# Kernel optimization log

Measured on AMD Instinct MI355X. Metric: run time of the kernel, lower is better.

Reference implementation:

```python
import jax, jax.numpy as jnp
import numpy as np

B, T, C = 8, 1024, 192


def _cluster_one(D, num_clusters):
    """Average-linkage agglomerative clustering on a precomputed [T,T] distance
    matrix (same algorithm as sklearn AgglomerativeClustering(metric='precomputed',
    linkage='average')). Returns int labels in [0, num_clusters)."""
    Tn = D.shape[0]
    INF = jnp.float32(1e9)
    eye = jnp.eye(Tn, dtype=bool)

    def body(_, state):
        D, labels, sizes, active = state
        mask = active[:, None] & active[None, :] & (~eye)
        Dm = jnp.where(mask, D, INF)
        flat = jnp.argmin(Dm)            # closest active pair
        i, j = flat // Tn, flat % Tn     # merge cluster j into cluster i
        ni, nj = sizes[i], sizes[j]
        # average linkage: d(i∪j, k) = (ni*d(i,k) + nj*d(j,k)) / (ni+nj)
        new_row = (ni * D[i] + nj * D[j]) / (ni + nj)
        D = D.at[i, :].set(new_row).at[:, i].set(new_row)
        sizes = sizes.at[i].set(ni + nj)
        active = active.at[j].set(False)
        labels = jnp.where(labels == j, i, labels)
        return (D, labels, sizes, active)

    state0 = (D,
              jnp.arange(Tn),
              jnp.ones((Tn,), jnp.float32),
              jnp.ones((Tn,), bool))
    n_merges = Tn - num_clusters  # static Python int -> static trip count
    D, labels, sizes, active = jax.lax.fori_loop(0, n_merges, body, state0)
    # compact representative indices to labels 0..num_clusters-1 (ordered by rep index)
    reps_sorted = jnp.sort(jnp.where(active, jnp.arange(Tn), Tn))
    return jnp.searchsorted(reps_sorted, labels)


def setup_inputs() -> dict:
    key = jax.random.key(0)
    x = jax.random.normal(key, (B, T, C), dtype=jnp.float32)
    return {"x": x, "num_clusters": 196}


def reference(x, num_clusters):
    num_clusters = min(int(num_clusters), x.shape[1])  # protected = 0
    xn = x / jnp.linalg.norm(x, axis=-1, keepdims=True)
    dist = 1.0 - jnp.einsum('btc,bsc->bts', xn, xn)    # [B,T,T] cosine distance
    labels = jax.vmap(lambda d: _cluster_one(d, num_clusters))(dist)
    return dist, labels
```

## Files before the change

### kernel.cpp

```cpp
#include <hip/hip_runtime.h>
#include <stdint.h>

#define TN 1024
#define CD 192
#define NB 8
#define WPB 16
#define NWG (NB * WPB)
#define NCLUST 196
#define NMERGE (TN - NCLUST)
#define TAILN 168
#define PCAP 64
#define NROUNDS 16
#define HIMASK 0xFFFFFFFF00000000ull

typedef unsigned long long ull;

__device__ __forceinline__ uint32_t f2sort(float f) {
    uint32_t u = __float_as_uint(f);
    return u ^ ((u >> 31) ? 0xFFFFFFFFu : 0x80000000u);
}

template<int CTRL>
__device__ __forceinline__ ull dpp_min64(ull x) {
    int lo = (int)(uint32_t)x, hi = (int)(uint32_t)(x >> 32);
    int tlo = __builtin_amdgcn_update_dpp(lo, lo, CTRL, 0xF, 0xF, false);
    int thi = __builtin_amdgcn_update_dpp(hi, hi, CTRL, 0xF, 0xF, false);
    ull t = ((ull)(uint32_t)thi << 32) | (uint32_t)tlo;
    return (t < x) ? t : x;
}
__device__ __forceinline__ ull wmin64_all(ull x) {
    x = dpp_min64<0x111>(x); x = dpp_min64<0x112>(x);
    x = dpp_min64<0x114>(x); x = dpp_min64<0x118>(x);
    x = dpp_min64<0x142>(x); x = dpp_min64<0x143>(x);
    int lo = __builtin_amdgcn_readlane((int)(uint32_t)x, 63);
    int hi = __builtin_amdgcn_readlane((int)(uint32_t)(x >> 32), 63);
    return ((ull)(uint32_t)hi << 32) | (uint32_t)lo;
}

__global__ void norm_kernel(const float* __restrict__ x, float* __restrict__ xn) {
    int row = blockIdx.x;
    int t = threadIdx.x;
    __shared__ float ssum[4];
    float v = 0.f;
    if (t < CD) v = x[(size_t)row * CD + t];
    float s = v * v;
    #pragma unroll
    for (int off = 32; off > 0; off >>= 1) s += __shfl_xor(s, off, 64);
    if ((t & 63) == 0) ssum[t >> 6] = s;
    __syncthreads();
    float tot = ssum[0] + ssum[1] + ssum[2] + ssum[3];
    float nrm = __fsqrt_rn(tot);
    if (t < CD) xn[(size_t)row * CD + t] = __fdiv_rn(v, nrm);
}

#define KC 32
__global__ __launch_bounds__(256) void dist_kernel(const float* __restrict__ xn,
                                                   float* __restrict__ dout) {
    int b = blockIdx.z;
    int bm = blockIdx.y, bn = blockIdx.x;
    const float* X = xn + (size_t)b * TN * CD;
    __shared__ float As[KC][68];
    __shared__ float Bs[KC][68];
    int tid = threadIdx.x;
    int tx = tid & 15, ty = tid >> 4;
    int lr = tid >> 2;
    int lq = tid & 3;
    float acc[4][4];
    #pragma unroll
    for (int r = 0; r < 4; ++r)
        #pragma unroll
        for (int c = 0; c < 4; ++c) acc[r][c] = 0.f;

    for (int kc = 0; kc < CD; kc += KC) {
        float4 a0 = *(const float4*)&X[(size_t)(bm * 64 + lr) * CD + kc + lq * 4];
        float4 a1 = *(const float4*)&X[(size_t)(bm * 64 + lr) * CD + kc + (lq + 4) * 4];
        float4 b0 = *(const float4*)&X[(size_t)(bn * 64 + lr) * CD + kc + lq * 4];
        float4 b1 = *(const float4*)&X[(size_t)(bn * 64 + lr) * CD + kc + (lq + 4) * 4];
        __syncthreads();
        As[lq * 4 + 0][lr] = a0.x; As[lq * 4 + 1][lr] = a0.y;
        As[lq * 4 + 2][lr] = a0.z; As[lq * 4 + 3][lr] = a0.w;
        As[lq * 4 + 16][lr] = a1.x; As[lq * 4 + 17][lr] = a1.y;
        As[lq * 4 + 18][lr] = a1.z; As[lq * 4 + 19][lr] = a1.w;
        Bs[lq * 4 + 0][lr] = b0.x; Bs[lq * 4 + 1][lr] = b0.y;
        Bs[lq * 4 + 2][lr] = b0.z; Bs[lq * 4 + 3][lr] = b0.w;
        Bs[lq * 4 + 16][lr] = b1.x; Bs[lq * 4 + 17][lr] = b1.y;
        Bs[lq * 4 + 18][lr] = b1.z; Bs[lq * 4 + 19][lr] = b1.w;
        __syncthreads();
        #pragma unroll
        for (int kk = 0; kk < KC; ++kk) {
            float4 av = *(const float4*)&As[kk][ty * 4];
            float4 bv = *(const float4*)&Bs[kk][tx * 4];
            acc[0][0] += av.x * bv.x; acc[0][1] += av.x * bv.y;
            acc[0][2] += av.x * bv.z; acc[0][3] += av.x * bv.w;
            acc[1][0] += av.y * bv.x; acc[1][1] += av.y * bv.y;
            acc[1][2] += av.y * bv.z; acc[1][3] += av.y * bv.w;
            acc[2][0] += av.z * bv.x; acc[2][1] += av.z * bv.y;
            acc[2][2] += av.z * bv.z; acc[2][3] += av.z * bv.w;
            acc[3][0] += av.w * bv.x; acc[3][1] += av.w * bv.y;
            acc[3][2] += av.w * bv.z; acc[3][3] += av.w * bv.w;
        }
    }
    size_t obase = (size_t)b * TN * TN;
    #pragma unroll
    for (int r = 0; r < 4; ++r) {
        int mrow = bm * 64 + ty * 4 + r;
        float4 o;
        o.x = 1.0f - acc[r][0]; o.y = 1.0f - acc[r][1];
        o.z = 1.0f - acc[r][2]; o.w = 1.0f - acc[r][3];
        size_t idx = obase + (size_t)mrow * TN + bn * 64 + tx * 4;
        *(float4*)&dout[idx] = o;
    }
}

__global__ __launch_bounds__(1024)
void init_kernel(const float* __restrict__ Dist, ull* __restrict__ rkg2,
                 float* __restrict__ szg2, int* __restrict__ gidg2,
                 ull* __restrict__ mkg, int* __restrict__ metag2) {
    int b = blockIdx.x >> 4;
    int w = blockIdx.x & 15;
    int k = threadIdx.x;
    int lane = k & 63, wv = k >> 6;
    int gw = w * 16 + wv;
    const float* D0 = Dist + (size_t)b * TN * TN;
    for (int r = gw; r < TN; r += 256) {
        const float* Rr = D0 + (size_t)r * TN;
        ull best = ~0ull;
        for (int s = lane; s < TN; s += 64)
            if (s != r) {
                ull key = ((ull)f2sort(Rr[s]) << 32) | (uint32_t)s;
                if (key < best) best = key;
            }
        best = wmin64_all(best);
        if (lane == 0) rkg2[(size_t)b * TN + r] = best;
    }
    if (w == 0) {
        szg2[b * TN + k] = 1.0f;
        gidg2[b * TN + k] = k;
        mkg[(size_t)b * TN + k] = ~0ull;
        if (k == 0) {
            metag2[b * 4 + 0] = TN;
            metag2[b * 4 + 1] = 0;
            metag2[b * 4 + 2] = 0;
        }
    }
}

__global__ __launch_bounds__(1024)
void round_kernel(int round, const float* __restrict__ Dinit,
                  float* __restrict__ DA, float* __restrict__ DB,
                  ull* __restrict__ rkg2, float* __restrict__ szg2,
                  int* __restrict__ gidg2, ull* __restrict__ mkg,
                  int* __restrict__ metag2) {
    int wg = blockIdx.x;
    int b = wg % NB;
    int w = wg / NB;
    int k = threadIdx.x;
    int lane = k & 63, wv = k >> 6;
    int gw = w * 16 + wv;
    int par = round & 1;

    const int* meta = metag2 + par * NB * 4 + b * 4;
    int N = meta[0], nm = meta[1], which = meta[2];

    if (N <= TAILN) {
        if (w == 0) {
            if (k < N) {
                szg2[(par ^ 1) * NB * TN + b * TN + k] = szg2[par * NB * TN + b * TN + k];
                gidg2[(par ^ 1) * NB * TN + b * TN + k] = gidg2[par * NB * TN + b * TN + k];
            }
            if (k == 0) {
                int* m2 = metag2 + (par ^ 1) * NB * 4 + b * 4;
                m2[0] = N; m2[1] = nm; m2[2] = which;
            }
        }
        return;
    }

    __shared__ ull rk_s[TN];
    __shared__ float sz_s[TN];
    __shared__ int gid_s[TN];
    __shared__ int ts_s[TN];
    __shared__ int n2o_s[TN];
    __shared__ unsigned char dead_s[TN];
    __shared__ int pi_t[512], pj_t[512];
    __shared__ ull pk_t[512];
    __shared__ int spi_s[512], spj_s[512];
    __shared__ int wcnt[16], woffp[16];
    __shared__ int npair_s;

    if (k < N) {
        rk_s[k] = rkg2[(size_t)par * NB * TN + (size_t)b * TN + k];
        sz_s[k] = szg2[par * NB * TN + b * TN + k];
        gid_s[k] = gidg2[par * NB * TN + b * TN + k];
    }
    ts_s[k] = -1;
    dead_s[k] = 0;
    __syncthreads();

    bool mut = false; int cpart = 0;
    if (k < N) {
        ull K = rk_s[k];
        int c = (int)(uint32_t)K;
        if ((int)(uint32_t)rk_s[c] == k && k < c) { mut = true; cpart = c; }
    }
    ull bm = __ballot(mut);
    int lanepre = __popcll(bm & (((ull)1 << lane) - 1ull));
    if (lane == 0) wcnt[wv] = __popcll(bm);
    __syncthreads();
    if (k == 0) {
        int run = 0;
        #pragma unroll
        for (int u = 0; u < 16; ++u) { woffp[u] = run; run += wcnt[u]; }
        npair_s = run;
    }
    __syncthreads();
    if (mut) { int idx = woffp[wv] + lanepre; pi_t[idx] = k; pj_t[idx] = cpart; }
    __syncthreads();
    int np = npair_s;
    if (np == 0) {
        ull cand = ~0ull;
        if (k < N) cand = (rk_s[k] & HIMASK) | (uint32_t)k;
        cand = wmin64_all(cand);
        if (lane == 0) pk_t[wv] = cand;
        __syncthreads();
        if (k == 0) {
            ull g = pk_t[0];
            for (int u = 1; u < 16; ++u) if (pk_t[u] < g) g = pk_t[u];
            int r = (int)(uint32_t)g;
            int c = (int)(uint32_t)rk_s[r];
            pi_t[0] = r < c ? r : c;
            pj_t[0] = r < c ? c : r;
            npair_s = 1;
        }
        __syncthreads();
        np = 1;
    }
    if (k < np) {
        int i = pi_t[k], j = pj_t[k];
        uint32_t vb = (uint32_t)(rk_s[i] >> 32);
        pk_t[k] = ((ull)vb << 20) | ((ull)(uint32_t)gid_s[i] << 10) | (ull)(uint32_t)gid_s[j];
    }
    __syncthreads();
    if (k < np) {
        ull mk = pk_t[k];
        int rank = 0;
        for (int u = 0; u < np; ++u) if (pk_t[u] < mk) ++rank;
        spi_s[rank] = pi_t[k]; spj_s[rank] = pj_t[k];
        if (w == 0) mkg[(size_t)b * TN + nm + rank] = mk;
    }
    __syncthreads();
    if (k < np) { ts_s[spi_s[k]] = k; dead_s[spj_s[k]] = 1; }
    __syncthreads();
    bool alive_ = (k < N) && !dead_s[k];
    ull am = __ballot(alive_);
    int apre = __popcll(am & (((ull)1 << lane) - 1ull));
    if (lane == 0) wcnt[wv] = __popcll(am);
    __syncthreads();
    if (k == 0) {
        int run = 0;
        #pragma unroll
        for (int u = 0; u < 16; ++u) { woffp[u] = run; run += wcnt[u]; }
    }
    __syncthreads();
    if (alive_) n2o_s[woffp[wv] + apre] = k;
    int Nn = N - np;
    __syncthreads();

    const float* cur = (which == 0) ? (Dinit + (size_t)b * TN * TN)
                      : ((which == 1) ? DA : DB) + (size_t)b * TN * TN;
    float* nxt = ((which == 1) ? DB : DA) + (size_t)b * TN * TN;
    int newwhich = (which == 1) ? 2 : 1;

    for (int ap = gw; ap < Nn; ap += 256) {
        int a = n2o_s[ap];
        int qa = ts_s[a];
        float* drow = nxt + (size_t)ap * Nn;
        ull best = ~0ull;
        if (qa < 0) {
            const float* Ra = cur + (size_t)a * N;
            for (int bp = lane; bp < Nn; bp += 64) {
                int bo = n2o_s[bp];
                int qb = ts_s[bo];
                float val;
                if (qb < 0) val = Ra[bo];
                else {
                    int iq = spi_s[qb], jq = spj_s[qb];
                    float niq = sz_s[iq], njq = sz_s[jq];
                    float sq = __fadd_rn(niq, njq);
                    val = __fdiv_rn(__fadd_rn(__fmul_rn(niq, Ra[iq]),
                                              __fmul_rn(njq, Ra[jq])), sq);
                }
                drow[bp] = val;
                if (bp != ap) {
                    ull key = ((ull)f2sort(val) << 32) | (uint32_t)bp;
                    if (key < best) best = key;
                }
            }
        } else {
            int ii = spi_s[qa], jj = spj_s[qa];
            float ni = sz_s[ii], nj = sz_s[jj], ss = __fadd_rn(ni, nj);
            const float* Ri = cur + (size_t)ii * N;
            const float* Rj = cur + (size_t)jj * N;
            for (int bp = lane; bp < Nn; bp += 64) {
                int bo = n2o_s[bp];
                int qb = ts_s[bo];
                float val;
                if (qb < 0) {
                    val = __fdiv_rn(__fadd_rn(__fmul_rn(ni, Ri[bo]),
                                              __fmul_rn(nj, Rj[bo])), ss);
                } else if (qb == qa) {
                    val = 0.0f;
                } else {
                    int p = qa < qb ? qa : qb, q2 = qa < qb ? qb : qa;
                    int ip = spi_s[p], jp = spj_s[p], iq = spi_s[q2], jq = spj_s[q2];
                    float nip = sz_s[ip], njp = sz_s[jp], sp = __fadd_rn(nip, njp);
                    float niq = sz_s[iq], njq = sz_s[jq], sq = __fadd_rn(niq, njq);
                    float t1 = __fdiv_rn(__fadd_rn(__fmul_rn(nip, cur[(size_t)ip * N + iq]),
                                                   __fmul_rn(njp, cur[(size_t)jp * N + iq])), sp);
                    float t2 = __fdiv_rn(__fadd_rn(__fmul_rn(nip, cur[(size_t)ip * N + jq]),
                                                   __fmul_rn(njp, cur[(size_t)jp * N + jq])), sp);
                    val = __fdiv_rn(__fadd_rn(__fmul_rn(niq, t1), __fmul_rn(njq, t2)), sq);
                }
                drow[bp] = val;
                if (bp != ap) {
                    ull key = ((ull)f2sort(val) << 32) | (uint32_t)bp;
                    if (key < best) best = key;
                }
            }
        }
        best = wmin64_all(best);
        if (lane == 0) rkg2[(size_t)(par ^ 1) * NB * TN + (size_t)b * TN + ap] = best;
    }

    if (w == 0) {
        if (k < Nn) {
            int a = n2o_s[k]; int q = ts_s[a];
            float ns = (q >= 0) ? __fadd_rn(sz_s[spi_s[q]], sz_s[spj_s[q]]) : sz_s[a];
            szg2[(par ^ 1) * NB * TN + b * TN + k] = ns;
            gidg2[(par ^ 1) * NB * TN + b * TN + k] = gid_s[a];
        }
        if (k == 0) {
            int* m2 = metag2 + (par ^ 1) * NB * 4 + b * 4;
            m2[0] = Nn; m2[1] = nm + np; m2[2] = newwhich;
        }
    }
}

__global__ __launch_bounds__(1024)
void tail_kernel(int fpar, const float* __restrict__ DA, const float* __restrict__ DB,
                 const float* __restrict__ szg2, const int* __restrict__ gidg2,
                 const ull* __restrict__ mkg, const int* __restrict__ metag2,
                 float* __restrict__ out_labels) {
    int b = blockIdx.x;
    int k = threadIdx.x;
    int lane = k & 63, wv = k >> 6;

    __shared__ float Dl[TAILN * TAILN];
    __shared__ ull rk_s[TAILN];
    __shared__ float sz_s[TAILN];
    __shared__ int gid_s[TAILN];
    __shared__ unsigned char alive[TAILN];
    __shared__ int tsl[TAILN];
    __shared__ float F[PCAP * PCAP];
    __shared__ int pi_t[96], pj_t[96];
    __shared__ ull pk_t[96];
    __shared__ int spi_s[PCAP], spj_s[PCAP];
    __shared__ ull mk_s[TN];
    __shared__ int par_s[TN];
    __shared__ uint32_t rw[32];
    __shared__ int woff2[32];
    __shared__ ull wpA[16];
    __shared__ int npair_s;

    int N = metag2[fpar * NB * 4 + b * 4 + 0];
    int nm = metag2[fpar * NB * 4 + b * 4 + 1];
    int which = metag2[fpar * NB * 4 + b * 4 + 2];
    const float* src = ((which == 1) ? DA : DB) + (size_t)b * TN * TN;

    for (int idx = k; idx < N * N; idx += 1024) Dl[idx] = src[idx];
    mk_s[k] = mkg[(size_t)b * TN + k];
    if (k < N) {
        sz_s[k] = szg2[fpar * NB * TN + b * TN + k];
        gid_s[k] = gidg2[fpar * NB * TN + b * TN + k];
        alive[k] = 1;
        tsl[k] = -1;
    }
    __syncthreads();

    int na = N;
    for (int round = 0; round < 600 && na > 1; ++round) {
        for (int r = wv; r < N; r += 16) {
            ull best = ~0ull;
            if (alive[r]) {
                for (int s = lane; s < N; s += 64)
                    if (alive[s] && s != r) {
                        ull key = ((ull)f2sort(Dl[r * N + s]) << 32) | (uint32_t)s;
                        if (key < best) best = key;
                    }
                best = wmin64_all(best);
            }
            if (lane == 0) rk_s[r] = best;
        }
        if (k == 0) npair_s = 0;
        __syncthreads();
        if (k < N && alive[k]) {
            ull K = rk_s[k];
            int c = (int)(uint32_t)K;
            if ((int)(uint32_t)rk_s[c] == k && k < c) {
                int idx = atomicAdd(&npair_s, 1);
                pi_t[idx] = k; pj_t[idx] = c;
            }
        }
        __syncthreads();
        int np = npair_s;
        if (np == 0) {
            ull cand = ~0ull;
            if (k < N && alive[k]) cand = (rk_s[k] & HIMASK) | (uint32_t)k;
            cand = wmin64_all(cand);
            if (lane == 0) wpA[wv] = cand;
            __syncthreads();
            if (k == 0) {
                ull g = wpA[0];
                for (int u = 1; u < 16; ++u) if (wpA[u] < g) g = wpA[u];
                int r = (int)(uint32_t)g;
                int c = (int)(uint32_t)rk_s[r];
                pi_t[0] = r < c ? r : c;
                pj_t[0] = r < c ? c : r;
                npair_s = 1;
            }
            __syncthreads();
            np = 1;
        }
        int P = np < PCAP ? np : PCAP;
        if (k < np) {
            int i = pi_t[k], j = pj_t[k];
            uint32_t vb = (uint32_t)(rk_s[i] >> 32);
            pk_t[k] = ((ull)vb << 20) | ((ull)(uint32_t)gid_s[i] << 10) | (ull)(uint32_t)gid_s[j];
        }
        __syncthreads();
        if (k < np) {
            ull mk = pk_t[k];
            int rank = 0;
            for (int u = 0; u < np; ++u) if (pk_t[u] < mk) ++rank;
            if (rank < P) { spi_s[rank] = pi_t[k]; spj_s[rank] = pj_t[k]; mk_s[nm + rank] = mk; }
        }
        __syncthreads();
        for (int t = k; t < P * P; t += 1024) {
            int p = t / P, q = t - p * P;
            if (p < q) {
                int ip = spi_s[p], jp = spj_s[p], iq = spi_s[q], jq = spj_s[q];
                float nip = sz_s[ip], njp = sz_s[jp], sp = __fadd_rn(nip, njp);
                float niq = sz_s[iq], njq = sz_s[jq], sq = __fadd_rn(niq, njq);
                float t1 = __fdiv_rn(__fadd_rn(__fmul_rn(nip, Dl[ip * N + iq]),
                                               __fmul_rn(njp, Dl[jp * N + iq])), sp);
                float t2 = __fdiv_rn(__fadd_rn(__fmul_rn(nip, Dl[ip * N + jq]),
                                               __fmul_rn(njp, Dl[jp * N + jq])), sp);
                F[p * PCAP + q] = __fdiv_rn(__fadd_rn(__fmul_rn(niq, t1), __fmul_rn(njq, t2)), sq);
            }
        }
        if (k < P) { tsl[spi_s[k]] = k; alive[spj_s[k]] = 0; }
        __syncthreads();
        for (int q = wv; q < P; q += 16) {
            int ii = spi_s[q], jj = spj_s[q];
            float ni = sz_s[ii], nj = sz_s[jj], ss = __fadd_rn(ni, nj);
            for (int s = lane; s < N; s += 64) {
                if (!alive[s] || s == ii) continue;
                int tp = tsl[s];
                float val;
                if (tp >= 0) {
                    int p2 = tp < q ? tp : q, q2 = tp < q ? q : tp;
                    val = F[p2 * PCAP + q2];
                } else {
                    val = __fdiv_rn(__fadd_rn(__fmul_rn(ni, Dl[ii * N + s]),
                                              __fmul_rn(nj, Dl[jj * N + s])), ss);
                }
                Dl[ii * N + s] = val;
                Dl[s * N + ii] = val;
            }
        }
        __syncthreads();
        if (k < P) {
            int ii = spi_s[k];
            sz_s[ii] = __fadd_rn(sz_s[ii], sz_s[spj_s[k]]);
            tsl[ii] = -1;
        }
        nm += P;
        na -= P;
        __syncthreads();
    }

    __syncthreads();
    par_s[k] = k;
    if (k < 32) rw[k] = 0;
    __syncthreads();
    if (k < TN - 1) {
        ull mk = mk_s[k];
        if (mk != ~0ull) {
            int rank = 0;
            for (int u = 0; u < TN - 1; ++u) if (mk_s[u] < mk) ++rank;
            if (rank < NMERGE) {
                int jj = (int)(mk & 1023ull);
                int ii = (int)((mk >> 10) & 1023ull);
                par_s[jj] = ii;
            }
        }
    }
    __syncthreads();
    #pragma unroll
    for (int it = 0; it < 11; ++it) {
        int p1 = par_s[k];
        int g = par_s[p1];
        __syncthreads();
        par_s[k] = g;
        __syncthreads();
    }
    if (par_s[k] == k) atomicOr(&rw[k >> 5], 1u << (k & 31));
    __syncthreads();
    if (k == 0) {
        int run = 0;
        for (int u = 0; u < 32; ++u) { woff2[u] = run; run += __popc(rw[u]); }
    }
    __syncthreads();
    int p = par_s[k];
    int rank = woff2[p >> 5] + __popc(rw[p >> 5] & ((1u << (p & 31)) - 1u));
    out_labels[(size_t)b * TN + k] = (float)rank;
}

extern "C" void kernel_launch(void* const* d_in, const int* in_sizes, int n_in,
                              void* d_out, int out_size, void* d_ws, size_t ws_size,
                              hipStream_t stream) {
    const float* x = (const float*)d_in[0];
    float* out = (float*)d_out;

    float* xn    = (float*)d_ws;
    float* DAp   = xn + (size_t)NB * TN * CD;
    float* DBp   = DAp + (size_t)NB * TN * TN;
    ull*   rkg2  = (ull*)(DBp + (size_t)NB * TN * TN);
    float* szg2  = (float*)(rkg2 + 2 * (size_t)NB * TN);
    int*   gidg2 = (int*)(szg2 + 2 * (size_t)NB * TN);
    ull*   mkg   = (ull*)(gidg2 + 2 * (size_t)NB * TN);
    int*   metag2 = (int*)(mkg + (size_t)NB * TN);

    float* dist_out   = out;
    float* labels_out = out + (size_t)NB * TN * TN;

    norm_kernel<<<NB * TN, 256, 0, stream>>>(x, xn);
    dim3 g2(16, 16, NB);
    dist_kernel<<<g2, 256, 0, stream>>>(xn, dist_out);
    init_kernel<<<NWG, 1024, 0, stream>>>(dist_out, rkg2, szg2, gidg2, mkg, metag2);
    for (int r = 0; r < NROUNDS; ++r)
        round_kernel<<<NWG, 1024, 0, stream>>>(r, dist_out, DAp, DBp,
                                               rkg2, szg2, gidg2, mkg, metag2);
    tail_kernel<<<NB, 1024, 0, stream>>>(NROUNDS & 1, DAp, DBp, szg2, gidg2,
                                         mkg, metag2, labels_out);
}
```

Measured before the change: 453.7 us.

## Shrink tail threshold and use radix select for merge-key ranking

```diff
diff --git a/kernel.cpp b/kernel.cpp
--- a/kernel.cpp
+++ b/kernel.cpp
@@ -9,8 +9,9 @@
 #define NCLUST 196
 #define NMERGE (TN - NCLUST)
 #define TAILN 168
+#define HSTOP 64
 #define PCAP 64
-#define NROUNDS 16
+#define NROUNDS 14
 #define HIMASK 0xFFFFFFFF00000000ull
 
 typedef unsigned long long ull;
@@ -162,7 +163,7 @@
     const int* meta = metag2 + par * NB * 4 + b * 4;
     int N = meta[0], nm = meta[1], which = meta[2];
 
-    if (N <= TAILN) {
+    if (N <= HSTOP) {
         if (w == 0) {
             if (k < N) {
                 szg2[(par ^ 1) * NB * TN + b * TN + k] = szg2[par * NB * TN + b * TN + k];
@@ -371,6 +372,9 @@
     __shared__ int woff2[32];
     __shared__ ull wpA[16];
     __shared__ int npair_s;
+    __shared__ int hist[256];
+    __shared__ ull chosen_sh;
+    __shared__ int target_sh;
 
     int N = metag2[fpar * NB * 4 + b * 4 + 0];
     int nm = metag2[fpar * NB * 4 + b * 4 + 1];
@@ -492,18 +496,33 @@
     __syncthreads();
     par_s[k] = k;
     if (k < 32) rw[k] = 0;
-    __syncthreads();
-    if (k < TN - 1) {
-        ull mk = mk_s[k];
-        if (mk != ~0ull) {
-            int rank = 0;
-            for (int u = 0; u < TN - 1; ++u) if (mk_s[u] < mk) ++rank;
-            if (rank < NMERGE) {
-                int jj = (int)(mk & 1023ull);
-                int ii = (int)((mk >> 10) & 1023ull);
-                par_s[jj] = ii;
-            }
-        }
+    if (k == 0) { chosen_sh = 0; target_sh = NMERGE - 1; }
+    __syncthreads();
+    ull myk = (k < TN - 1) ? mk_s[k] : ~0ull;
+    #pragma unroll
+    for (int pass = 6; pass >= 0; --pass) {
+        if (k < 256) hist[k] = 0;
+        __syncthreads();
+        int sh = pass * 8;
+        bool inset = (k < TN - 1) && ((myk >> (sh + 8)) == chosen_sh);
+        if (inset) atomicAdd(&hist[(int)((myk >> sh) & 255)], 1);
+        __syncthreads();
+        if (k == 0) {
+            int run = 0, t = target_sh, bs = 0;
+            for (int u = 0; u < 256; ++u) {
+                int c = hist[u];
+                if (t < run + c) { bs = u; t -= run; break; }
+                run += c;
+            }
+            target_sh = t;
+            chosen_sh = (chosen_sh << 8) | (ull)bs;
+        }
+        __syncthreads();
+    }
+    if (k < TN - 1 && myk <= chosen_sh) {
+        int jj = (int)(myk & 1023ull);
+        int ii = (int)((myk >> 10) & 1023ull);
+        par_s[jj] = ii;
     }
     __syncthreads();
     #pragma unroll
```

Result: slower. 466.2 us (+2.8%).

## Split tail into single-wave finish kernel and separate label kernel

Applied to the files above, without the earlier changes.

```diff
diff --git a/kernel.cpp b/kernel.cpp
--- a/kernel.cpp
+++ b/kernel.cpp
@@ -9,8 +9,9 @@
 #define NCLUST 196
 #define NMERGE (TN - NCLUST)
 #define TAILN 168
+#define HSTOP 64
 #define PCAP 64
-#define NROUNDS 16
+#define NROUNDS 14
 #define HIMASK 0xFFFFFFFF00000000ull
 
 typedef unsigned long long ull;
@@ -162,7 +163,7 @@
     const int* meta = metag2 + par * NB * 4 + b * 4;
     int N = meta[0], nm = meta[1], which = meta[2];
 
-    if (N <= TAILN) {
+    if (N <= HSTOP) {
         if (w == 0) {
             if (k < N) {
                 szg2[(par ^ 1) * NB * TN + b * TN + k] = szg2[par * NB * TN + b * TN + k];
@@ -346,14 +347,13 @@
     }
 }
 
-__global__ __launch_bounds__(1024)
-void tail_kernel(int fpar, const float* __restrict__ DA, const float* __restrict__ DB,
-                 const float* __restrict__ szg2, const int* __restrict__ gidg2,
-                 const ull* __restrict__ mkg, const int* __restrict__ metag2,
-                 float* __restrict__ out_labels) {
+#define WBAR() __builtin_amdgcn_wave_barrier()
+__global__ __launch_bounds__(64)
+void finish_kernel(int fpar, const float* __restrict__ DA, const float* __restrict__ DB,
+                   const float* __restrict__ szg2, const int* __restrict__ gidg2,
+                   ull* __restrict__ mkg, const int* __restrict__ metag2) {
     int b = blockIdx.x;
-    int k = threadIdx.x;
-    int lane = k & 63, wv = k >> 6;
+    int lane = threadIdx.x;
 
     __shared__ float Dl[TAILN * TAILN];
     __shared__ ull rk_s[TAILN];
@@ -365,87 +365,94 @@
     __shared__ int pi_t[96], pj_t[96];
     __shared__ ull pk_t[96];
     __shared__ int spi_s[PCAP], spj_s[PCAP];
-    __shared__ ull mk_s[TN];
-    __shared__ int par_s[TN];
-    __shared__ uint32_t rw[32];
-    __shared__ int woff2[32];
-    __shared__ ull wpA[16];
-    __shared__ int npair_s;
 
     int N = metag2[fpar * NB * 4 + b * 4 + 0];
     int nm = metag2[fpar * NB * 4 + b * 4 + 1];
     int which = metag2[fpar * NB * 4 + b * 4 + 2];
     const float* src = ((which == 1) ? DA : DB) + (size_t)b * TN * TN;
 
-    for (int idx = k; idx < N * N; idx += 1024) Dl[idx] = src[idx];
-    mk_s[k] = mkg[(size_t)b * TN + k];
-    if (k < N) {
-        sz_s[k] = szg2[fpar * NB * TN + b * TN + k];
-        gid_s[k] = gidg2[fpar * NB * TN + b * TN + k];
-        alive[k] = 1;
-        tsl[k] = -1;
-    }
-    __syncthreads();
+    for (int idx = lane; idx < N * N; idx += 64) Dl[idx] = src[idx];
+    for (int r = lane; r < N; r += 64) {
+        sz_s[r] = szg2[fpar * NB * TN + b * TN + r];
+        gid_s[r] = gidg2[fpar * NB * TN + b * TN + r];
+        alive[r] = 1;
+        tsl[r] = -1;
+    }
+    WBAR();
+    asm volatile("s_waitcnt vmcnt(0) lgkmcnt(0)" ::: "memory");
 
     int na = N;
-    for (int round = 0; round < 600 && na > 1; ++round) {
-        for (int r = wv; r < N; r += 16) {
-            ull best = ~0ull;
-            if (alive[r]) {
-                for (int s = lane; s < N; s += 64)
-                    if (alive[s] && s != r) {
-                        ull key = ((ull)f2sort(Dl[r * N + s]) << 32) | (uint32_t)s;
-                        if (key < best) best = key;
-                    }
-                best = wmin64_all(best);
-            }
-            if (lane == 0) rk_s[r] = best;
-        }
-        if (k == 0) npair_s = 0;
-        __syncthreads();
-        if (k < N && alive[k]) {
-            ull K = rk_s[k];
-            int c = (int)(uint32_t)K;
-            if ((int)(uint32_t)rk_s[c] == k && k < c) {
-                int idx = atomicAdd(&npair_s, 1);
-                pi_t[idx] = k; pj_t[idx] = c;
-            }
-        }
-        __syncthreads();
-        int np = npair_s;
+    while (na > 1) {
+        #pragma unroll
+        for (int rr = 0; rr < 3; ++rr) {
+            int r = lane + rr * 64;
+            if (r < N) {
+                ull best = ~0ull;
+                if (alive[r]) {
+                    for (int s = 0; s < N; ++s)
+                        if (alive[s] && s != r) {
+                            ull key = ((ull)f2sort(Dl[r * N + s]) << 32) | (uint32_t)s;
+                            if (key < best) best = key;
+                        }
+                }
+                rk_s[r] = best;
+            }
+        }
+        WBAR();
+        int np = 0;
+        #pragma unroll
+        for (int rr = 0; rr < 3; ++rr) {
+            int r = lane + rr * 64;
+            bool mut = false; int c = 0;
+            if (r < N && alive[r]) {
+                ull K = rk_s[r];
+                if (K != ~0ull) {
+                    c = (int)(uint32_t)K;
+                    ull Kc = rk_s[c];
+                    if ((int)(uint32_t)Kc == r && r < c) mut = true;
+                }
+            }
+            ull bmm = __ballot(mut);
+            int pre = __popcll(bmm & (((ull)1 << lane) - 1ull));
+            if (mut) { pi_t[np + pre] = r; pj_t[np + pre] = c; }
+            np += (int)__popcll(bmm);
+        }
+        WBAR();
         if (np == 0) {
             ull cand = ~0ull;
-            if (k < N && alive[k]) cand = (rk_s[k] & HIMASK) | (uint32_t)k;
-            cand = wmin64_all(cand);
-            if (lane == 0) wpA[wv] = cand;
-            __syncthreads();
-            if (k == 0) {
-                ull g = wpA[0];
-                for (int u = 1; u < 16; ++u) if (wpA[u] < g) g = wpA[u];
-                int r = (int)(uint32_t)g;
-                int c = (int)(uint32_t)rk_s[r];
-                pi_t[0] = r < c ? r : c;
-                pj_t[0] = r < c ? c : r;
-                npair_s = 1;
-            }
-            __syncthreads();
+            #pragma unroll
+            for (int rr = 0; rr < 3; ++rr) {
+                int r = lane + rr * 64;
+                if (r < N && alive[r] && rk_s[r] != ~0ull) {
+                    ull c2 = (rk_s[r] & HIMASK) | (uint32_t)r;
+                    if (c2 < cand) cand = c2;
+                }
+            }
+            ull g = wmin64_all(cand);
+            int r = (int)(uint32_t)g;
+            int c = (int)(uint32_t)rk_s[r];
+            if (lane == 0) { pi_t[0] = r < c ? r : c; pj_t[0] = r < c ? c : r; }
             np = 1;
+            WBAR();
         }
         int P = np < PCAP ? np : PCAP;
-        if (k < np) {
-            int i = pi_t[k], j = pj_t[k];
+        for (int p = lane; p < np; p += 64) {
+            int i = pi_t[p], j = pj_t[p];
             uint32_t vb = (uint32_t)(rk_s[i] >> 32);
-            pk_t[k] = ((ull)vb << 20) | ((ull)(uint32_t)gid_s[i] << 10) | (ull)(uint32_t)gid_s[j];
-        }
-        __syncthreads();
-        if (k < np) {
-            ull mk = pk_t[k];
+            pk_t[p] = ((ull)vb << 20) | ((ull)(uint32_t)gid_s[i] << 10) | (ull)(uint32_t)gid_s[j];
+        }
+        WBAR();
+        for (int p = lane; p < np; p += 64) {
+            ull mk = pk_t[p];
             int rank = 0;
             for (int u = 0; u < np; ++u) if (pk_t[u] < mk) ++rank;
-            if (rank < P) { spi_s[rank] = pi_t[k]; spj_s[rank] = pj_t[k]; mk_s[nm + rank] = mk; }
-        }
-        __syncthreads();
-        for (int t = k; t < P * P; t += 1024) {
+            if (rank < P) {
+                spi_s[rank] = pi_t[p]; spj_s[rank] = pj_t[p];
+                mkg[(size_t)b * TN + nm + rank] = mk;
+            }
+        }
+        WBAR();
+        for (int t = lane; t < P * P; t += 64) {
             int p = t / P, q = t - p * P;
             if (p < q) {
                 int ip = spi_s[p], jp = spj_s[p], iq = spi_s[q], jq = spj_s[q];
@@ -458,9 +465,9 @@
                 F[p * PCAP + q] = __fdiv_rn(__fadd_rn(__fmul_rn(niq, t1), __fmul_rn(njq, t2)), sq);
             }
         }
-        if (k < P) { tsl[spi_s[k]] = k; alive[spj_s[k]] = 0; }
-        __syncthreads();
-        for (int q = wv; q < P; q += 16) {
+        for (int p = lane; p < P; p += 64) { tsl[spi_s[p]] = p; alive[spj_s[p]] = 0; }
+        WBAR();
+        for (int q = 0; q < P; ++q) {
             int ii = spi_s[q], jj = spj_s[q];
             float ni = sz_s[ii], nj = sz_s[jj], ss = __fadd_rn(ni, nj);
             for (int s = lane; s < N; s += 64) {
@@ -478,18 +485,28 @@
                 Dl[s * N + ii] = val;
             }
         }
-        __syncthreads();
-        if (k < P) {
-            int ii = spi_s[k];
-            sz_s[ii] = __fadd_rn(sz_s[ii], sz_s[spj_s[k]]);
+        WBAR();
+        for (int p = lane; p < P; p += 64) {
+            int ii = spi_s[p];
+            sz_s[ii] = __fadd_rn(sz_s[ii], sz_s[spj_s[p]]);
             tsl[ii] = -1;
         }
         nm += P;
         na -= P;
-        __syncthreads();
-    }
-
-    __syncthreads();
+        WBAR();
+    }
+}
+
+__global__ __launch_bounds__(1024)
+void label_kernel(const ull* __restrict__ mkg, float* __restrict__ out_labels) {
+    int b = blockIdx.x;
+    int k = threadIdx.x;
+    __shared__ ull mk_s[TN];
+    __shared__ int par_s[TN];
+    __shared__ uint32_t rw[32];
+    __shared__ int woff2[32];
+
+    mk_s[k] = mkg[(size_t)b * TN + k];
     par_s[k] = k;
     if (k < 32) rw[k] = 0;
     __syncthreads();
@@ -551,6 +568,7 @@
     for (int r = 0; r < NROUNDS; ++r)
         round_kernel<<<NWG, 1024, 0, stream>>>(r, dist_out, DAp, DBp,
                                                rkg2, szg2, gidg2, mkg, metag2);
-    tail_kernel<<<NB, 1024, 0, stream>>>(NROUNDS & 1, DAp, DBp, szg2, gidg2,
-                                         mkg, metag2, labels_out);
-}
+    finish_kernel<<<NB, 64, 0, stream>>>(NROUNDS & 1, DAp, DBp, szg2, gidg2,
+                                         mkg, metag2);
+    label_kernel<<<NB, 1024, 0, stream>>>(mkg, labels_out);
+}
```

Result: slower. 909.4 us (+100.4%).
